# Kernel tuning notes

Hardware: AMD Instinct MI355X
Metric: run time of the kernel (lower is better)

The kernel has to match this reference:

```python
import jax, jax.numpy as jnp
import numpy as np

G, N, F_IN = 1024, 256, 128
HID = [256, 256, 256]
KS = [32, 16, 8]
N_OUT = 2


def _graph_conv(adj, x, W, b, act):
    # DGL GraphConv, norm='both': h = D^{-1/2} A D^{-1/2} X W + b
    deg = adj.sum(-1)                                   # [G, n]
    norm = jax.lax.rsqrt(jnp.maximum(deg, 1.0))[..., None]
    h = (x * norm) @ W                                  # [G, n, d_out]
    h = jnp.einsum('gnm,gmd->gnd', adj, h) * norm + b
    return act(h) if act is not None else h


def _sag_pool(adj, x, Ws, bs, k):
    # SAGPool: score via GraphConv, keep top-k nodes, gate by tanh(score),
    # take induced subgraph adjacency.
    score = _graph_conv(adj, x, Ws, bs, None)[..., 0]   # [G, n]
    sv, idx = jax.lax.top_k(score, k)                   # [G, k]
    x_sel = jnp.take_along_axis(x, idx[:, :, None], axis=1) * jnp.tanh(sv)[:, :, None]
    a = jnp.take_along_axis(adj, idx[:, :, None], axis=1)
    a = jnp.take_along_axis(a, idx[:, None, :], axis=2)  # [G, k, k]
    return a, x_sel


def _sum_max_readout(x):
    return jnp.concatenate([x.sum(axis=1), x.max(axis=1)], axis=-1)  # [G, 2d]


def setup_inputs() -> dict:
    key = jax.random.key(0)
    ks = jax.random.split(key, 16)
    feat = jax.random.normal(ks[0], (G, N, F_IN), dtype=jnp.float32)
    # sparse-ish symmetric binary adjacency, avg degree ~ 16
    a = (jax.random.uniform(ks[1], (G, N, N)) < (16.0 / N)).astype(jnp.float32)
    adj = jnp.maximum(a, jnp.swapaxes(a, 1, 2))

    def glorot(k, shp):
        lim = float(np.sqrt(6.0 / (shp[0] + shp[1])))
        return jax.random.uniform(k, shp, jnp.float32, -lim, lim)

    dims = [F_IN] + HID
    inp = {'feat': feat, 'adj': adj}
    for i in range(3):
        inp[f'W{i}'] = glorot(ks[2 + i], (dims[i], dims[i + 1]))
        inp[f'b{i}'] = jnp.zeros((dims[i + 1],), jnp.float32)
        inp[f'Ws{i}'] = glorot(ks[5 + i], (dims[i + 1], 1))
        inp[f'bs{i}'] = jnp.zeros((1,), jnp.float32)
    inp['Wd1'] = glorot(ks[8], (2 * sum(HID), 128))
    inp['bd1'] = jnp.zeros((128,), jnp.float32)
    inp['Wd2'] = glorot(ks[9], (128, N_OUT))
    inp['bd2'] = jnp.zeros((N_OUT,), jnp.float32)
    return inp


def reference(feat, adj, W0, b0, Ws0, bs0, W1, b1, Ws1, bs1, W2, b2, Ws2, bs2,
              Wd1, bd1, Wd2, bd2):
    act = jax.nn.leaky_relu  # F.leaky_relu, slope 0.01
    Wgs = [(W0, b0), (W1, b1), (W2, b2)]
    Wss = [(Ws0, bs0), (Ws1, bs1), (Ws2, bs2)]
    readouts = []
    x, a = feat, adj
    for i in range(3):
        x = _graph_conv(a, x, Wgs[i][0], Wgs[i][1], act)
        a, x = _sag_pool(a, x, Wss[i][0], Wss[i][1], KS[i])
        readouts.append(_sum_max_readout(x))
    merged = jnp.concatenate(readouts, axis=1)          # [G, 2*sum(HID)]
    # dropout omitted (deterministic eval reference)
    h = act(merged @ Wd1 + bd1)
    out = jax.nn.sigmoid(h @ Wd2 + bd2)                 # [G, n_output]
    return out
```

## Files before the change

### kernel.cpp

```cpp
#include <hip/hip_runtime.h>
#include <math.h>

constexpr int GG  = 1024;
constexpr int NN  = 256;
constexpr int FF  = 128;
constexpr int DD  = 256;
constexpr int KS0 = 32, KS1 = 16, KS2 = 8;

__device__ __forceinline__ float lrelu(float x){ return x >= 0.f ? x : 0.01f*x; }

__device__ __forceinline__ unsigned short f2bf(float f) {
  unsigned u = __float_as_uint(f);
  unsigned r = (u + 0x7FFFu + ((u >> 16) & 1u)) >> 16;
  return (unsigned short)r;
}
__device__ __forceinline__ float bf2f(unsigned short h) {
  return __uint_as_float(((unsigned)h) << 16);
}

typedef __attribute__((ext_vector_type(8)))  __bf16 bf16x8;
typedef __attribute__((ext_vector_type(16))) float  f32x16;

union Frag8 { unsigned short us[8]; unsigned long long u64[2]; bf16x8 v; };

typedef __attribute__((address_space(1))) void gvoid;
typedef __attribute__((address_space(3))) void lvoid;
__device__ __forceinline__ void async_cp16(const unsigned short* g, unsigned short* l) {
  __builtin_amdgcn_global_load_lds((const gvoid*)g, (lvoid*)l, 16, 0, 0);
}

__global__ void k_splitW_all(const float* __restrict__ Wa, const float* __restrict__ Wb,
                             const float* __restrict__ Wc,
                             unsigned short* __restrict__ oa, unsigned short* __restrict__ ob,
                             unsigned short* __restrict__ oc) {
  int e = blockIdx.x*256 + threadIdx.x;
  if (e >= FF*DD + 2*DD*DD) return;
  const float* W; unsigned short* out; int K;
  if (e < FF*DD)                { W = Wa; out = oa; K = FF; }
  else if (e < FF*DD + DD*DD)   { e -= FF*DD; W = Wb; out = ob; K = DD; }
  else                          { e -= FF*DD + DD*DD; W = Wc; out = oc; K = DD; }
  int j    = e & 7;
  int lane = (e >> 3) & 63;
  int nt   = (e >> 9) & 7;
  int s    = (e >> 12) & 1;
  int kti  = e >> 13;
  int n = nt*32 + (lane & 31);
  int k = kti*32 + s*16 + ((lane >> 5) << 3) + j;
  float x = W[(size_t)k*DD + n];
  unsigned short h1 = f2bf(x);  float r1 = x - bf2f(h1);
  unsigned short h2 = f2bf(r1); float r2 = r1 - bf2f(h2);
  unsigned short h3 = f2bf(r2);
  out[e] = h1; out[DD*K + e] = h2; out[2*DD*K + e] = h3;
}

__global__ void k_maskrow(const float* __restrict__ adj, float* __restrict__ norm0,
                          unsigned long long* __restrict__ mask) {
  int row = blockIdx.x*4 + (threadIdx.x >> 6);
  int lane = threadIdx.x & 63;
  const float* ar = adj + (size_t)row*NN;
  float f0 = ar[lane], f1 = ar[64 + lane], f2 = ar[128 + lane], f3 = ar[192 + lane];
  unsigned long long m0 = __ballot(f0 > 0.5f);
  unsigned long long m1 = __ballot(f1 > 0.5f);
  unsigned long long m2 = __ballot(f2 > 0.5f);
  unsigned long long m3 = __ballot(f3 > 0.5f);
  if (lane < 4) {
    unsigned long long mm = lane == 0 ? m0 : lane == 1 ? m1 : lane == 2 ? m2 : m3;
    mask[(size_t)row*4 + lane] = mm;
  }
  if (lane == 0) {
    int cnt = __popcll(m0) + __popcll(m1) + __popcll(m2) + __popcll(m3);
    norm0[row] = rsqrtf(fmaxf((float)cnt, 1.0f));
  }
}

constexpr int QS = 68;
__global__ __launch_bounds__(256, 2) void k_spmm_f(
    const float* __restrict__ feat, const unsigned long long* __restrict__ mask,
    const float* __restrict__ norm0, float* __restrict__ T0) {
  __shared__ unsigned short ls[3*128*QS];
  __shared__ float snorm[NN];

  int g = blockIdx.x;
  int t = threadIdx.x;
  int lane = t & 63, wave = t >> 6;
  int lm = lane & 31, lh = lane >> 5;

  const float* Xg = feat + (size_t)g*NN*FF;

  snorm[t] = norm0[g*NN + t];

  unsigned long long mrow[2][4];
  #pragma unroll
  for (int mt = 0; mt < 2; ++mt) {
    const unsigned long long* mp = mask + ((size_t)g*NN + wave*64 + mt*32 + lm)*4;
    #pragma unroll
    for (int w = 0; w < 4; ++w) mrow[mt][w] = mp[w];
  }

  f32x16 acc[2][4];
  #pragma unroll
  for (int i = 0; i < 2; ++i)
    #pragma unroll
    for (int j = 0; j < 4; ++j) acc[i][j] = (f32x16)0.0f;

  __syncthreads();

  for (int kq = 0; kq < 4; ++kq) {
    #pragma unroll
    for (int i = 0; i < 8; ++i) {
      int g2 = t + i*256;
      int c  = g2 & 127;
      int mg = g2 >> 7;
      int m0 = kq*64 + mg*4;
      unsigned long long p1 = 0, p2 = 0, p3 = 0;
      #pragma unroll
      for (int jj = 0; jj < 4; ++jj) {
        float x = Xg[(size_t)(m0 + jj)*FF + c] * snorm[m0 + jj];
        unsigned short h1 = f2bf(x);  float r1 = x - bf2f(h1);
        unsigned short h2 = f2bf(r1); float r2 = r1 - bf2f(h2);
        unsigned short h3 = f2bf(r2);
        p1 |= (unsigned long long)h1 << (16*jj);
        p2 |= (unsigned long long)h2 << (16*jj);
        p3 |= (unsigned long long)h3 << (16*jj);
      }
      int base = c*QS + mg*4;
      *reinterpret_cast<unsigned long long*>(&ls[base])            = p1;
      *reinterpret_cast<unsigned long long*>(&ls[128*QS + base])   = p2;
      *reinterpret_cast<unsigned long long*>(&ls[2*128*QS + base]) = p3;
    }
    __syncthreads();

    #pragma unroll
    for (int ktq = 0; ktq < 2; ++ktq) {
      Frag8 afr[2][2];
      #pragma unroll
      for (int mt = 0; mt < 2; ++mt)
        #pragma unroll
        for (int s = 0; s < 2; ++s) {
          int shift = ktq*32 + s*16 + lh*8;
          unsigned byte = (unsigned)(mrow[mt][kq] >> shift) & 0xFFu;
          #pragma unroll
          for (int j = 0; j < 8; ++j)
            afr[mt][s].us[j] = ((byte >> j) & 1u) ? (unsigned short)0x3F80 : (unsigned short)0;
        }
      #pragma unroll
      for (int s = 0; s < 2; ++s)
        #pragma unroll
        for (int nt = 0; nt < 4; ++nt) {
          int kk = ktq*32 + s*16 + lh*8;
          int base = (nt*32 + lm)*QS + kk;
          Frag8 b0_, b1_, b2_;
          b0_.v = *reinterpret_cast<const bf16x8*>(&ls[base]);
          b1_.v = *reinterpret_cast<const bf16x8*>(&ls[128*QS + base]);
          b2_.v = *reinterpret_cast<const bf16x8*>(&ls[2*128*QS + base]);
          #pragma unroll
          for (int mt = 0; mt < 2; ++mt) {
            acc[mt][nt] = __builtin_amdgcn_mfma_f32_32x32x16_bf16(afr[mt][s].v, b0_.v, acc[mt][nt], 0,0,0);
            acc[mt][nt] = __builtin_amdgcn_mfma_f32_32x32x16_bf16(afr[mt][s].v, b1_.v, acc[mt][nt], 0,0,0);
            acc[mt][nt] = __builtin_amdgcn_mfma_f32_32x32x16_bf16(afr[mt][s].v, b2_.v, acc[mt][nt], 0,0,0);
          }
        }
    }
    __syncthreads();
  }

  #pragma unroll
  for (int mt = 0; mt < 2; ++mt)
    #pragma unroll
    for (int nt = 0; nt < 4; ++nt)
      #pragma unroll
      for (int r = 0; r < 16; ++r) {
        int row = wave*64 + mt*32 + (r & 3) + 8*(r >> 2) + 4*lh;
        int col = nt*32 + lm;
        T0[((size_t)g*NN + row)*FF + col] = acc[mt][nt][r];
      }
}

__global__ __launch_bounds__(256, 2) void k_gemm0(
    const float* __restrict__ Tmat, const unsigned short* __restrict__ Wk,
    const float* __restrict__ normv, const float* __restrict__ bias,
    const float* __restrict__ Ws, float* __restrict__ hs) {
  __shared__ unsigned short bsh[3*8192];
  int t = threadIdx.x;
  int lane = t & 63, wave = t >> 6;
  int lm = lane & 31, lh = lane >> 5;
  int rowbase = blockIdx.x*128 + wave*32;

  f32x16 acc[8];
  #pragma unroll
  for (int nt = 0; nt < 8; ++nt) acc[nt] = (f32x16)0.0f;

  for (int kti = 0; kti < 4; ++kti) {
    int kt = kti*32;
    float4 af[2][2];
    #pragma unroll
    for (int s = 0; s < 2; ++s) {
      const float* ap = Tmat + (size_t)(rowbase + lm)*FF + kt + s*16 + lh*8;
      af[s][0] = *reinterpret_cast<const float4*>(ap);
      af[s][1] = *reinterpret_cast<const float4*>(ap + 4);
    }
    __syncthreads();
    #pragma unroll
    for (int sp = 0; sp < 3; ++sp)
      #pragma unroll
      for (int r = 0; r < 4; ++r) {
        const unsigned short* src = Wk + (size_t)sp*DD*FF + (size_t)kti*8192 + r*2048 + t*8;
        unsigned short* dst = bsh + sp*8192 + r*2048 + t*8;
        async_cp16(src, dst);
      }
    __syncthreads();
    Frag8 afr[2][3];
    #pragma unroll
    for (int s = 0; s < 2; ++s) {
      const float* fv = &af[s][0].x;
      #pragma unroll
      for (int j = 0; j < 8; ++j) {
        float x = fv[j];
        unsigned short h1 = f2bf(x);  float r1 = x - bf2f(h1);
        unsigned short h2 = f2bf(r1); float r2 = r1 - bf2f(h2);
        afr[s][0].us[j] = h1; afr[s][1].us[j] = h2; afr[s][2].us[j] = f2bf(r2);
      }
    }
    #pragma unroll
    for (int s = 0; s < 2; ++s)
      #pragma unroll
      for (int nt = 0; nt < 8; ++nt) {
        const unsigned short* bp = bsh + ((s*8 + nt)*64 + lane)*8;
        Frag8 b0_, b1_, b2_;
        b0_.v = *reinterpret_cast<const bf16x8*>(bp);
        b1_.v = *reinterpret_cast<const bf16x8*>(bp + 8192);
        b2_.v = *reinterpret_cast<const bf16x8*>(bp + 16384);
        acc[nt] = __builtin_amdgcn_mfma_f32_32x32x16_bf16(afr[s][0].v, b0_.v, acc[nt], 0,0,0);
        acc[nt] = __builtin_amdgcn_mfma_f32_32x32x16_bf16(afr[s][0].v, b1_.v, acc[nt], 0,0,0);
        acc[nt] = __builtin_amdgcn_mfma_f32_32x32x16_bf16(afr[s][1].v, b0_.v, acc[nt], 0,0,0);
        acc[nt] = __builtin_amdgcn_mfma_f32_32x32x16_bf16(afr[s][0].v, b2_.v, acc[nt], 0,0,0);
        acc[nt] = __builtin_amdgcn_mfma_f32_32x32x16_bf16(afr[s][2].v, b0_.v, acc[nt], 0,0,0);
        acc[nt] = __builtin_amdgcn_mfma_f32_32x32x16_bf16(afr[s][1].v, b1_.v, acc[nt], 0,0,0);
      }
  }

  float bcol[8], wcol[8];
  #pragma unroll
  for (int nt = 0; nt < 8; ++nt) { int col = nt*32 + lm; bcol[nt] = bias[col]; wcol[nt] = Ws[col]; }
  float hsum[16];
  #pragma unroll
  for (int r = 0; r < 16; ++r) {
    int row = rowbase + (r & 3) + 8*(r >> 2) + 4*lh;
    float nv = normv[row];
    float hp = 0.f;
    #pragma unroll
    for (int nt = 0; nt < 8; ++nt) hp += lrelu(nv*acc[nt][r] + bcol[nt])*wcol[nt];
    hsum[r] = hp;
  }
  #pragma unroll
  for (int off = 1; off <= 16; off <<= 1)
    #pragma unroll
    for (int r = 0; r < 16; ++r) hsum[r] += __shfl_xor(hsum[r], off);
  if (lm == 0)
    #pragma unroll
    for (int r = 0; r < 16; ++r) {
      int row = rowbase + (r & 3) + 8*(r >> 2) + 4*lh;
      hs[row] = normv[row]*hsum[r];
    }
}

__global__ __launch_bounds__(256) void k_topk_sel0(
    const unsigned long long* __restrict__ mask, const float* __restrict__ hs,
    const float* __restrict__ norm0, const float* __restrict__ bs,
    const float* __restrict__ T0, const float* __restrict__ W0,
    const float* __restrict__ b0, float* __restrict__ x_sel,
    float* __restrict__ a1, float* __restrict__ merged) {
  __shared__ float sh[NN];
  __shared__ float ssc[NN];
  __shared__ float sT[KS0*FF];
  __shared__ int sidx[KS0]; __shared__ float stv[KS0]; __shared__ float snv[KS0];
  int g = blockIdx.x, t = threadIdx.x;

  sh[t] = hs[g*NN + t];
  __syncthreads();
  const unsigned long long* mr = mask + ((size_t)g*NN + t)*4;
  float s = 0.f;
  #pragma unroll
  for (int w = 0; w < 4; ++w) {
    unsigned long long m = mr[w];
    const float* base = sh + w*64;
    while (m) {
      int c = __builtin_ctzll(m);
      s += base[c];
      m &= m - 1;
    }
  }
  ssc[t] = norm0[g*NN + t]*s + bs[0];
  __syncthreads();
  if (t < 64) {
    float sv[4]; int si[4];
    #pragma unroll
    for (int e = 0; e < 4; ++e) { sv[e] = ssc[e*64 + t]; si[e] = e*64 + t; }
    for (int kk = 0; kk < KS0; ++kk) {
      float bs_ = -INFINITY; int bi = 1 << 30;
      #pragma unroll
      for (int e = 0; e < 4; ++e)
        if (sv[e] > bs_ || (sv[e] == bs_ && si[e] < bi)) { bs_ = sv[e]; bi = si[e]; }
      for (int off = 32; off; off >>= 1) {
        float os = __shfl_xor(bs_, off);
        int oi = __shfl_xor(bi, off);
        if (os > bs_ || (os == bs_ && oi < bi)) { bs_ = os; bi = oi; }
      }
      if (t == 0) { sidx[kk] = bi; stv[kk] = tanhf(bs_); }
      #pragma unroll
      for (int e = 0; e < 4; ++e) if (si[e] == bi) sv[e] = -INFINITY;
    }
  }
  __syncthreads();
  if (t < KS0) snv[t] = norm0[g*NN + sidx[t]];
  #pragma unroll
  for (int i = 0; i < 4; ++i) {
    int e4 = t + i*256;
    int r = e4 >> 5, c4 = e4 & 31;
    reinterpret_cast<float4*>(sT)[e4] =
        *reinterpret_cast<const float4*>(&T0[((size_t)g*NN + sidx[r])*FF + c4*4]);
  }
  __syncthreads();
  float sum[KS0];
  #pragma unroll
  for (int j = 0; j < KS0; ++j) sum[j] = 0.f;
  for (int k = 0; k < FF; k += 4) {
    float4 w;
    w.x = W0[(size_t)(k+0)*DD + t]; w.y = W0[(size_t)(k+1)*DD + t];
    w.z = W0[(size_t)(k+2)*DD + t]; w.w = W0[(size_t)(k+3)*DD + t];
    #pragma unroll
    for (int j = 0; j < KS0; ++j) {
      float4 tv4 = *reinterpret_cast<const float4*>(&sT[j*FF + k]);
      sum[j] += tv4.x*w.x + tv4.y*w.y + tv4.z*w.z + tv4.w*w.w;
    }
  }
  float b = b0[t];
  float ssum = 0.f, mx = -INFINITY;
  #pragma unroll
  for (int j = 0; j < KS0; ++j) {
    float val = lrelu(snv[j]*sum[j] + b) * stv[j];
    x_sel[((size_t)g*KS0 + j)*DD + t] = val;
    ssum += val; mx = fmaxf(mx, val);
  }
  merged[(size_t)g*1536 + t] = ssum;
  merged[(size_t)g*1536 + 256 + t] = mx;
  for (int e = t; e < KS0*KS0; e += 256) {
    int r = e >> 5, c = e & 31;
    int nr = sidx[r], nc = sidx[c];
    unsigned long long m = mask[((size_t)g*NN + nr)*4 + (nc >> 6)];
    a1[(size_t)g*KS0*KS0 + e] = (float)((m >> (nc & 63)) & 1ull);
  }
}

__global__ __launch_bounds__(256, 2) void k_fused1(
    const float* __restrict__ a, const float* __restrict__ xin,
    const unsigned short* __restrict__ Wk, const float* __restrict__ bias,
    const float* __restrict__ Ws, const float* __restrict__ bs,
    float* __restrict__ x_sel_out, float* __restrict__ a_out,
    float* __restrict__ merged) {
  constexpr int n = KS0;
  constexpr int kp = KS1;
  constexpr int TP = DD + 4;
  __shared__ float sa[n*n];
  __shared__ float bufA[n*DD];
  __shared__ float sT[n*TP];
  __shared__ float snorm[n]; __shared__ float shs[n]; __shared__ float ssc[n];
  __shared__ int sidx[kp]; __shared__ float stv[kp];
  int g = blockIdx.x, t = threadIdx.x;
  int lane = t & 63, wave = t >> 6, lm = lane & 31, lh = lane >> 5;

  for (int e = t; e < n*n; e += 256) sa[e] = a[(size_t)g*n*n + e];
  __syncthreads();
  if (t < n) {
    float dg = 0.f;
    for (int m = 0; m < n; ++m) dg += sa[m*n + t];
    snorm[t] = rsqrtf(fmaxf(dg, 1.f));
  }
  __syncthreads();
  {
    const float4* xp = reinterpret_cast<const float4*>(xin + (size_t)g*n*DD);
    #pragma unroll
    for (int i = 0; i < (n*DD/4)/256; ++i) {
      int e4 = t + i*256;
      float4 v = xp[e4];
      float nv = snorm[e4 >> 6];
      v.x *= nv; v.y *= nv; v.z *= nv; v.w *= nv;
      reinterpret_cast<float4*>(bufA)[e4] = v;
    }
  }
  __syncthreads();
  {
    float acc2[n];
    #pragma unroll
    for (int r = 0; r < n; ++r) acc2[r] = 0.f;
    for (int m = 0; m < n; ++m) {
      float xv = bufA[m*DD + t];
      #pragma unroll
      for (int r = 0; r < n; ++r) acc2[r] += sa[r*n + m]*xv;
    }
    #pragma unroll
    for (int r = 0; r < n; ++r) sT[r*TP + t] = acc2[r];
  }
  __syncthreads();

  f32x16 acc[2];
  acc[0] = (f32x16)0.0f; acc[1] = (f32x16)0.0f;
  for (int kti = 0; kti < DD/32; ++kti) {
    int kt = kti*32;
    Frag8 afr[2][3];
    #pragma unroll
    for (int s = 0; s < 2; ++s) {
      float4 af4[2];
      const float* ap = &sT[lm*TP + kt + s*16 + lh*8];
      af4[0] = *reinterpret_cast<const float4*>(ap);
      af4[1] = *reinterpret_cast<const float4*>(ap + 4);
      const float* fv = &af4[0].x;
      #pragma unroll
      for (int j = 0; j < 8; ++j) {
        float x = fv[j];
        unsigned short h1 = f2bf(x);  float r1 = x - bf2f(h1);
        unsigned short h2 = f2bf(r1); float r2 = r1 - bf2f(h2);
        afr[s][0].us[j] = h1; afr[s][1].us[j] = h2; afr[s][2].us[j] = f2bf(r2);
      }
    }
    #pragma unroll
    for (int s = 0; s < 2; ++s)
      #pragma unroll
      for (int ntl = 0; ntl < 2; ++ntl) {
        int ct = wave*2 + ntl;
        size_t boff = ((((size_t)kti*2 + s)*8 + ct)*64 + lane)*8;
        Frag8 b0_, b1_, b2_;
        b0_.v = *reinterpret_cast<const bf16x8*>(Wk + boff);
        b1_.v = *reinterpret_cast<const bf16x8*>(Wk + (size_t)DD*DD + boff);
        b2_.v = *reinterpret_cast<const bf16x8*>(Wk + (size_t)2*DD*DD + boff);
        acc[ntl] = __builtin_amdgcn_mfma_f32_32x32x16_bf16(afr[s][0].v, b0_.v, acc[ntl], 0,0,0);
        acc[ntl] = __builtin_amdgcn_mfma_f32_32x32x16_bf16(afr[s][0].v, b1_.v, acc[ntl], 0,0,0);
        acc[ntl] = __builtin_amdgcn_mfma_f32_32x32x16_bf16(afr[s][1].v, b0_.v, acc[ntl], 0,0,0);
        acc[ntl] = __builtin_amdgcn_mfma_f32_32x32x16_bf16(afr[s][0].v, b2_.v, acc[ntl], 0,0,0);
        acc[ntl] = __builtin_amdgcn_mfma_f32_32x32x16_bf16(afr[s][2].v, b0_.v, acc[ntl], 0,0,0);
        acc[ntl] = __builtin_amdgcn_mfma_f32_32x32x16_bf16(afr[s][1].v, b1_.v, acc[ntl], 0,0,0);
      }
  }

  #pragma unroll
  for (int ntl = 0; ntl < 2; ++ntl) {
    int colbase = wave*64 + ntl*32 + lm;
    float bc = bias[colbase];
    #pragma unroll
    for (int r = 0; r < 16; ++r) {
      int row = (r & 3) + 8*(r >> 2) + 4*lh;
      bufA[row*DD + colbase] = lrelu(snorm[row]*acc[ntl][r] + bc);
    }
  }
  __syncthreads();
  if (wave == 0) {
    float wcol[8];
    #pragma unroll
    for (int nt = 0; nt < 8; ++nt) wcol[nt] = Ws[nt*32 + lm];
    float hsum[16];
    #pragma unroll
    for (int r = 0; r < 16; ++r) {
      int row = (r & 3) + 8*(r >> 2) + 4*lh;
      float hp = 0.f;
      #pragma unroll
      for (int nt = 0; nt < 8; ++nt) hp += bufA[row*DD + nt*32 + lm]*wcol[nt];
      hsum[r] = hp;
    }
    #pragma unroll
    for (int off = 1; off <= 16; off <<= 1)
      #pragma unroll
      for (int r = 0; r < 16; ++r) hsum[r] += __shfl_xor(hsum[r], off);
    if (lm == 0)
      #pragma unroll
      for (int r = 0; r < 16; ++r) {
        int row = (r & 3) + 8*(r >> 2) + 4*lh;
        shs[row] = snorm[row]*hsum[r];
      }
  }
  __syncthreads();
  if (t < n) {
    float s = 0.f;
    for (int m = 0; m < n; ++m) s += sa[m*n + t]*shs[m];
    ssc[t] = snorm[t]*s + bs[0];
  }
  __syncthreads();
  if (t < 64) {
    float sc = (t < n) ? ssc[t] : -INFINITY;
    int si = (t < n) ? t : (1 << 30);
    for (int kk = 0; kk < kp; ++kk) {
      float bs_ = sc; int bi = si;
      for (int off = 32; off; off >>= 1) {
        float os = __shfl_xor(bs_, off);
        int oi = __shfl_xor(bi, off);
        if (os > bs_ || (os == bs_ && oi < bi)) { bs_ = os; bi = oi; }
      }
      if (t == 0) { sidx[kk] = bi; stv[kk] = tanhf(bs_); }
      if (si == bi) sc = -INFINITY;
    }
  }
  __syncthreads();
  float sum = 0.f, mx = -INFINITY;
  #pragma unroll
  for (int j = 0; j < kp; ++j) {
    float v = bufA[sidx[j]*DD + t] * stv[j];
    x_sel_out[((size_t)g*kp + j)*DD + t] = v;
    sum += v; mx = fmaxf(mx, v);
  }
  merged[(size_t)g*1536 + 512 + t] = sum;
  merged[(size_t)g*1536 + 768 + t] = mx;
  { int r = t >> 4, c = t & 15;
    a_out[(size_t)g*kp*kp + t] = sa[sidx[r]*n + sidx[c]]; }
}

__global__ __launch_bounds__(256, 2) void k_fused2(
    const float* __restrict__ a, const float* __restrict__ xin,
    const unsigned short* __restrict__ Wk, const float* __restrict__ bias,
    const float* __restrict__ Ws, const float* __restrict__ bs,
    float* __restrict__ merged) {
  constexpr int n = KS1;
  constexpr int kp = KS2;
  constexpr int TP = DD + 4;
  __shared__ float sa[n*n];
  __shared__ float bufA[n*DD];
  __shared__ float sT[n*TP];
  __shared__ float snorm[n]; __shared__ float shs[n]; __shared__ float ssc[n];
  __shared__ int sidx[kp]; __shared__ float stv[kp];
  int g = blockIdx.x, t = threadIdx.x;
  int lane = t & 63, wave = t >> 6, lm = lane & 31, lh = lane >> 5;

  for (int e = t; e < n*n; e += 256) sa[e] = a[(size_t)g*n*n + e];
  __syncthreads();
  if (t < n) {
    float dg = 0.f;
    for (int m = 0; m < n; ++m) dg += sa[m*n + t];
    snorm[t] = rsqrtf(fmaxf(dg, 1.f));
  }
  __syncthreads();
  {
    const float4* xp = reinterpret_cast<const float4*>(xin + (size_t)g*n*DD);
    #pragma unroll
    for (int i = 0; i < (n*DD/4)/256; ++i) {
      int e4 = t + i*256;
      float4 v = xp[e4];
      float nv = snorm[e4 >> 6];
      v.x *= nv; v.y *= nv; v.z *= nv; v.w *= nv;
      reinterpret_cast<float4*>(bufA)[e4] = v;
    }
  }
  __syncthreads();
  {
    float acc2[n];
    #pragma unroll
    for (int r = 0; r < n; ++r) acc2[r] = 0.f;
    for (int m = 0; m < n; ++m) {
      float xv = bufA[m*DD + t];
      #pragma unroll
      for (int r = 0; r < n; ++r) acc2[r] += sa[r*n + m]*xv;
    }
    #pragma unroll
    for (int r = 0; r < n; ++r) sT[r*TP + t] = acc2[r];
  }
  __syncthreads();

  f32x16 acc[2];
  acc[0] = (f32x16)0.0f; acc[1] = (f32x16)0.0f;
  for (int kti = 0; kti < DD/32; ++kti) {
    int kt = kti*32;
    Frag8 afr[2][3];
    #pragma unroll
    for (int s = 0; s < 2; ++s) {
      float4 af4[2];
      if (lm < n) {
        const float* ap = &sT[lm*TP + kt + s*16 + lh*8];
        af4[0] = *reinterpret_cast<const float4*>(ap);
        af4[1] = *reinterpret_cast<const float4*>(ap + 4);
      } else {
        af4[0] = make_float4(0.f, 0.f, 0.f, 0.f);
        af4[1] = make_float4(0.f, 0.f, 0.f, 0.f);
      }
      const float* fv = &af4[0].x;
      #pragma unroll
      for (int j = 0; j < 8; ++j) {
        float x = fv[j];
        unsigned short h1 = f2bf(x);  float r1 = x - bf2f(h1);
        unsigned short h2 = f2bf(r1); float r2 = r1 - bf2f(h2);
        afr[s][0].us[j] = h1; afr[s][1].us[j] = h2; afr[s][2].us[j] = f2bf(r2);
      }
    }
    #pragma unroll
    for (int s = 0; s < 2; ++s)
      #pragma unroll
      for (int ntl = 0; ntl < 2; ++ntl) {
        int ct = wave*2 + ntl;
        size_t boff = ((((size_t)kti*2 + s)*8 + ct)*64 + lane)*8;
        Frag8 b0_, b1_, b2_;
        b0_.v = *reinterpret_cast<const bf16x8*>(Wk + boff);
        b1_.v = *reinterpret_cast<const bf16x8*>(Wk + (size_t)DD*DD + boff);
        b2_.v = *reinterpret_cast<const bf16x8*>(Wk + (size_t)2*DD*DD + boff);
        acc[ntl] = __builtin_amdgcn_mfma_f32_32x32x16_bf16(afr[s][0].v, b0_.v, acc[ntl], 0,0,0);
        acc[ntl] = __builtin_amdgcn_mfma_f32_32x32x16_bf16(afr[s][0].v, b1_.v, acc[ntl], 0,0,0);
        acc[ntl] = __builtin_amdgcn_mfma_f32_32x32x16_bf16(afr[s][1].v, b0_.v, acc[ntl], 0,0,0);
        acc[ntl] = __builtin_amdgcn_mfma_f32_32x32x16_bf16(afr[s][0].v, b2_.v, acc[ntl], 0,0,0);
        acc[ntl] = __builtin_amdgcn_mfma_f32_32x32x16_bf16(afr[s][2].v, b0_.v, acc[ntl], 0,0,0);
        acc[ntl] = __builtin_amdgcn_mfma_f32_32x32x16_bf16(afr[s][1].v, b1_.v, acc[ntl], 0,0,0);
      }
  }

  #pragma unroll
  for (int ntl = 0; ntl < 2; ++ntl) {
    int colbase = wave*64 + ntl*32 + lm;
    float bc = bias[colbase];
    #pragma unroll
    for (int r = 0; r < 16; ++r) {
      int row = (r & 3) + 8*(r >> 2) + 4*lh;
      if (row < n) bufA[row*DD + colbase] = lrelu(snorm[row]*acc[ntl][r] + bc);
    }
  }
  __syncthreads();
  if (wave == 0) {
    float wcol[8];
    #pragma unroll
    for (int nt = 0; nt < 8; ++nt) wcol[nt] = Ws[nt*32 + lm];
    float hsum[16];
    #pragma unroll
    for (int r = 0; r < 16; ++r) {
      int row = (r & 3) + 8*(r >> 2) + 4*lh;
      float hp = 0.f;
      if (row < n) {
        #pragma unroll
        for (int nt = 0; nt < 8; ++nt) hp += bufA[row*DD + nt*32 + lm]*wcol[nt];
      }
      hsum[r] = hp;
    }
    #pragma unroll
    for (int off = 1; off <= 16; off <<= 1)
      #pragma unroll
      for (int r = 0; r < 16; ++r) hsum[r] += __shfl_xor(hsum[r], off);
    if (lm == 0)
      #pragma unroll
      for (int r = 0; r < 16; ++r) {
        int row = (r & 3) + 8*(r >> 2) + 4*lh;
        if (row < n) shs[row] = snorm[row]*hsum[r];
      }
  }
  __syncthreads();
  if (t < n) {
    float s = 0.f;
    for (int m = 0; m < n; ++m) s += sa[m*n + t]*shs[m];
    ssc[t] = snorm[t]*s + bs[0];
  }
  __syncthreads();
  if (t < 64) {
    float sc = (t < n) ? ssc[t] : -INFINITY;
    int si = (t < n) ? t : (1 << 30);
    for (int kk = 0; kk < kp; ++kk) {
      float bs_ = sc; int bi = si;
      for (int off = 32; off; off >>= 1) {
        float os = __shfl_xor(bs_, off);
        int oi = __shfl_xor(bi, off);
        if (os > bs_ || (os == bs_ && oi < bi)) { bs_ = os; bi = oi; }
      }
      if (t == 0) { sidx[kk] = bi; stv[kk] = tanhf(bs_); }
      if (si == bi) sc = -INFINITY;
    }
  }
  __syncthreads();
  float sum = 0.f, mx = -INFINITY;
  #pragma unroll
  for (int j = 0; j < kp; ++j) {
    float v = bufA[sidx[j]*DD + t] * stv[j];
    sum += v; mx = fmaxf(mx, v);
  }
  merged[(size_t)g*1536 + 1024 + t] = sum;
  merged[(size_t)g*1536 + 1280 + t] = mx;
}

__global__ void k_mlp(const float* __restrict__ merged, const float* __restrict__ Wd1,
                      const float* __restrict__ bd1, const float* __restrict__ Wd2,
                      const float* __restrict__ bd2, float* __restrict__ out) {
  __shared__ float sm[4*1536];
  __shared__ float sh[4][128];
  int g0 = blockIdx.x*4; int t = threadIdx.x;
  for (int i = t; i < 4*1536; i += 128) sm[i] = merged[(size_t)g0*1536 + i];
  __syncthreads();
  float a0 = 0.f, a1 = 0.f, a2 = 0.f, a3 = 0.f;
  for (int kk = 0; kk < 1536; ++kk) {
    float w = Wd1[(size_t)kk*128 + t];
    a0 += sm[kk]*w; a1 += sm[1536 + kk]*w; a2 += sm[3072 + kk]*w; a3 += sm[4608 + kk]*w;
  }
  float b = bd1[t];
  sh[0][t] = lrelu(a0 + b); sh[1][t] = lrelu(a1 + b);
  sh[2][t] = lrelu(a2 + b); sh[3][t] = lrelu(a3 + b);
  __syncthreads();
  if (t < 8) {
    int gi = t >> 1, c = t & 1;
    float o = 0.f;
    for (int kk = 0; kk < 128; ++kk) o += sh[gi][kk]*Wd2[kk*2 + c];
    out[(size_t)(g0 + gi)*2 + c] = 1.f/(1.f + expf(-(o + bd2[c])));
  }
}

extern "C" void kernel_launch(void* const* d_in, const int* in_sizes, int n_in,
                              void* d_out, int out_size, void* d_ws, size_t ws_size,
                              hipStream_t stream) {
  const float* feat = (const float*)d_in[0];
  const float* adj  = (const float*)d_in[1];
  const float* W0 = (const float*)d_in[2];  const float* b0  = (const float*)d_in[3];
  const float* Ws0= (const float*)d_in[4];  const float* bs0 = (const float*)d_in[5];
  const float* W1 = (const float*)d_in[6];  const float* b1  = (const float*)d_in[7];
  const float* Ws1= (const float*)d_in[8];  const float* bs1 = (const float*)d_in[9];
  const float* W2 = (const float*)d_in[10]; const float* b2  = (const float*)d_in[11];
  const float* Ws2= (const float*)d_in[12]; const float* bs2 = (const float*)d_in[13];
  const float* Wd1= (const float*)d_in[14]; const float* bd1 = (const float*)d_in[15];
  const float* Wd2= (const float*)d_in[16]; const float* bd2 = (const float*)d_in[17];
  float* out = (float*)d_out;

  char* ws = (char*)d_ws;
  size_t off = 0;
  auto alloc = [&](size_t bytes) -> char* {
    char* p = ws + off; off += (bytes + 255) & ~(size_t)255; return p;
  };
  float* norm0 = (float*)alloc((size_t)GG*NN*4);
  unsigned long long* mask0 = (unsigned long long*)alloc((size_t)GG*NN*4*8);
  float* hs0   = (float*)alloc((size_t)GG*NN*4);
  float* merged= (float*)alloc((size_t)GG*1536*4);
  unsigned short* W0s = (unsigned short*)alloc((size_t)3*FF*DD*2);
  unsigned short* W1s = (unsigned short*)alloc((size_t)3*DD*DD*2);
  unsigned short* W2s = (unsigned short*)alloc((size_t)3*DD*DD*2);
  float* T0     = (float*)alloc((size_t)GG*NN*FF*4);
  float* x_sel1 = (float*)alloc((size_t)GG*KS0*DD*4);
  float* a1     = (float*)alloc((size_t)GG*KS0*KS0*4);
  float* x_sel2 = (float*)alloc((size_t)GG*KS1*DD*4);
  float* a2     = (float*)alloc((size_t)GG*KS1*KS1*4);

  k_splitW_all<<<(FF*DD + 2*DD*DD)/256, 256, 0, stream>>>(W0, W1, W2, W0s, W1s, W2s);

  k_maskrow<<<GG*NN/4, 256, 0, stream>>>(adj, norm0, mask0);
  k_spmm_f<<<GG, 256, 0, stream>>>(feat, mask0, norm0, T0);
  k_gemm0<<<GG*NN/128, 256, 0, stream>>>(T0, W0s, norm0, b0, Ws0, hs0);
  k_topk_sel0<<<GG, 256, 0, stream>>>(mask0, hs0, norm0, bs0, T0, W0, b0, x_sel1, a1, merged);

  k_fused1<<<GG, 256, 0, stream>>>(a1, x_sel1, W1s, b1, Ws1, bs1, x_sel2, a2, merged);

  k_fused2<<<GG, 256, 0, stream>>>(a2, x_sel2, W2s, b2, Ws2, bs2, merged);

  k_mlp<<<GG/4, 128, 0, stream>>>(merged, Wd1, bd1, Wd2, bd2, out);

  (void)in_sizes; (void)n_in; (void)out_size; (void)ws_size;
}
```

Baseline: 966.2 us.

## Replace dense bf16x3 MFMA aggregation with sparse bitmask-driven fp32 SpMM

The first-layer neighbor aggregation (A·D^-1/2·X) no longer runs as a dense 256x256 by 256x128 product on MFMA with a three-way bf16 split. Each thread now walks the set bits of its adjacency row mask and sums the normalized fp32 feature rows staged in shared memory. Work is split into two blocks per graph, each covering 64 feature columns. This exploits the sparsity (about 16 neighbors per row) to skip dense multiply work and the bf16 splitting, at the cost of data-dependent loop lengths that cause wave divergence and of scalar fp32 adds.

After: 947.9 us. No clear change (-1.9%).

```diff
diff --git a/kernel.cpp b/kernel.cpp
--- a/kernel.cpp
+++ b/kernel.cpp
@@ -73,107 +73,56 @@
   }
 }
 
-constexpr int QS = 68;
-__global__ __launch_bounds__(256, 2) void k_spmm_f(
+__global__ __launch_bounds__(256, 2) void k_spmm_s(
     const float* __restrict__ feat, const unsigned long long* __restrict__ mask,
     const float* __restrict__ norm0, float* __restrict__ T0) {
-  __shared__ unsigned short ls[3*128*QS];
+  constexpr int ST = 68;
+  __shared__ float ls[NN*ST];
   __shared__ float snorm[NN];
-
-  int g = blockIdx.x;
+  int bid = blockIdx.x;
+  int g = bid >> 1, half = bid & 1;
   int t = threadIdx.x;
-  int lane = t & 63, wave = t >> 6;
-  int lm = lane & 31, lh = lane >> 5;
-
-  const float* Xg = feat + (size_t)g*NN*FF;
+  const float* Xg = feat + (size_t)g*NN*FF + half*64;
 
   snorm[t] = norm0[g*NN + t];
-
-  unsigned long long mrow[2][4];
-  #pragma unroll
-  for (int mt = 0; mt < 2; ++mt) {
-    const unsigned long long* mp = mask + ((size_t)g*NN + wave*64 + mt*32 + lm)*4;
-    #pragma unroll
-    for (int w = 0; w < 4; ++w) mrow[mt][w] = mp[w];
-  }
-
-  f32x16 acc[2][4];
-  #pragma unroll
-  for (int i = 0; i < 2; ++i)
-    #pragma unroll
-    for (int j = 0; j < 4; ++j) acc[i][j] = (f32x16)0.0f;
-
-  __syncthreads();
-
-  for (int kq = 0; kq < 4; ++kq) {
-    #pragma unroll
-    for (int i = 0; i < 8; ++i) {
-      int g2 = t + i*256;
-      int c  = g2 & 127;
-      int mg = g2 >> 7;
-      int m0 = kq*64 + mg*4;
-      unsigned long long p1 = 0, p2 = 0, p3 = 0;
-      #pragma unroll
-      for (int jj = 0; jj < 4; ++jj) {
-        float x = Xg[(size_t)(m0 + jj)*FF + c] * snorm[m0 + jj];
-        unsigned short h1 = f2bf(x);  float r1 = x - bf2f(h1);
-        unsigned short h2 = f2bf(r1); float r2 = r1 - bf2f(h2);
-        unsigned short h3 = f2bf(r2);
-        p1 |= (unsigned long long)h1 << (16*jj);
-        p2 |= (unsigned long long)h2 << (16*jj);
-        p3 |= (unsigned long long)h3 << (16*jj);
-      }
-      int base = c*QS + mg*4;
-      *reinterpret_cast<unsigned long long*>(&ls[base])            = p1;
-      *reinterpret_cast<unsigned long long*>(&ls[128*QS + base])   = p2;
-      *reinterpret_cast<unsigned long long*>(&ls[2*128*QS + base]) = p3;
-    }
-    __syncthreads();
-
-    #pragma unroll
-    for (int ktq = 0; ktq < 2; ++ktq) {
-      Frag8 afr[2][2];
-      #pragma unroll
-      for (int mt = 0; mt < 2; ++mt)
-        #pragma unroll
-        for (int s = 0; s < 2; ++s) {
-          int shift = ktq*32 + s*16 + lh*8;
-          unsigned byte = (unsigned)(mrow[mt][kq] >> shift) & 0xFFu;
-          #pragma unroll
-          for (int j = 0; j < 8; ++j)
-            afr[mt][s].us[j] = ((byte >> j) & 1u) ? (unsigned short)0x3F80 : (unsigned short)0;
-        }
-      #pragma unroll
-      for (int s = 0; s < 2; ++s)
-        #pragma unroll
-        for (int nt = 0; nt < 4; ++nt) {
-          int kk = ktq*32 + s*16 + lh*8;
-          int base = (nt*32 + lm)*QS + kk;
-          Frag8 b0_, b1_, b2_;
-          b0_.v = *reinterpret_cast<const bf16x8*>(&ls[base]);
-          b1_.v = *reinterpret_cast<const bf16x8*>(&ls[128*QS + base]);
-          b2_.v = *reinterpret_cast<const bf16x8*>(&ls[2*128*QS + base]);
-          #pragma unroll
-          for (int mt = 0; mt < 2; ++mt) {
-            acc[mt][nt] = __builtin_amdgcn_mfma_f32_32x32x16_bf16(afr[mt][s].v, b0_.v, acc[mt][nt], 0,0,0);
-            acc[mt][nt] = __builtin_amdgcn_mfma_f32_32x32x16_bf16(afr[mt][s].v, b1_.v, acc[mt][nt], 0,0,0);
-            acc[mt][nt] = __builtin_amdgcn_mfma_f32_32x32x16_bf16(afr[mt][s].v, b2_.v, acc[mt][nt], 0,0,0);
-          }
-        }
-    }
-    __syncthreads();
-  }
-
-  #pragma unroll
-  for (int mt = 0; mt < 2; ++mt)
-    #pragma unroll
-    for (int nt = 0; nt < 4; ++nt)
-      #pragma unroll
-      for (int r = 0; r < 16; ++r) {
-        int row = wave*64 + mt*32 + (r & 3) + 8*(r >> 2) + 4*lh;
-        int col = nt*32 + lm;
-        T0[((size_t)g*NN + row)*FF + col] = acc[mt][nt][r];
-      }
+  const unsigned long long* mp = mask + ((size_t)g*NN + t)*4;
+  unsigned long long mrow[4];
+  #pragma unroll
+  for (int w = 0; w < 4; ++w) mrow[w] = mp[w];
+  __syncthreads();
+
+  #pragma unroll
+  for (int i = 0; i < 16; ++i) {
+    int e = t + i*256;
+    int r = e >> 4, c4 = (e & 15)*4;
+    float4 v = *reinterpret_cast<const float4*>(Xg + (size_t)r*FF + c4);
+    float nv = snorm[r];
+    v.x *= nv; v.y *= nv; v.z *= nv; v.w *= nv;
+    *reinterpret_cast<float4*>(&ls[r*ST + c4]) = v;
+  }
+  __syncthreads();
+
+  float4 acc[16];
+  #pragma unroll
+  for (int i = 0; i < 16; ++i) acc[i] = make_float4(0.f, 0.f, 0.f, 0.f);
+  #pragma unroll
+  for (int w = 0; w < 4; ++w) {
+    unsigned long long m = mrow[w];
+    while (m) {
+      int c = __builtin_ctzll(m);
+      const float4* xp = reinterpret_cast<const float4*>(&ls[(w*64 + c)*ST]);
+      #pragma unroll
+      for (int i = 0; i < 16; ++i) {
+        float4 v = xp[i];
+        acc[i].x += v.x; acc[i].y += v.y; acc[i].z += v.z; acc[i].w += v.w;
+      }
+      m &= m - 1;
+    }
+  }
+  float* op = T0 + ((size_t)g*NN + t)*FF + half*64;
+  #pragma unroll
+  for (int i = 0; i < 16; ++i)
+    *reinterpret_cast<float4*>(op + i*4) = acc[i];
 }
 
 __global__ __launch_bounds__(256, 2) void k_gemm0(
@@ -736,7 +685,7 @@
   k_splitW_all<<<(FF*DD + 2*DD*DD)/256, 256, 0, stream>>>(W0, W1, W2, W0s, W1s, W2s);
 
   k_maskrow<<<GG*NN/4, 256, 0, stream>>>(adj, norm0, mask0);
-  k_spmm_f<<<GG, 256, 0, stream>>>(feat, mask0, norm0, T0);
+  k_spmm_s<<<2*GG, 256, 0, stream>>>(feat, mask0, norm0, T0);
   k_gemm0<<<GG*NN/128, 256, 0, stream>>>(T0, W0s, norm0, b0, Ws0, hs0);
   k_topk_sel0<<<GG, 256, 0, stream>>>(mask0, hs0, norm0, bs0, T0, W0, b0, x_sel1, a1, merged);
 
```
